# Kernel tuning notes

Measured on AMD Instinct MI355X. Metric: run time of the kernel, lower is better.

Reference implementation:

```python
import jax, jax.numpy as jnp
import numpy as np

B, CIN, COUT, N, T, KT, DTEM, K, D = 16, 32, 64, 1024, 24, 3, 32, 8, 8
TOUT = T - (KT - 1) * 2  # dilated valid conv: 20
NEG = -32767.0  # -2**15 + 1, matches torch small_value


def conv1x1(x, w, b=None):
    # 1x1 Conv2d on NCHW-style [B, C, N, T]
    y = jnp.einsum('bcnt,oc->bont', x, w)
    return y if b is None else y + b[None, :, None, None]


def setup_inputs() -> dict:
    ks = jax.random.split(jax.random.key(0), 24)
    rn = lambda i, s, sc=0.1: jax.random.normal(ks[i], s, dtype=jnp.float32) * sc
    return {
        'x': rn(0, (B, CIN, N, T), 1.0),
        'tem_embedding': rn(1, (B, DTEM, N, T), 0.1),
        'A0': rn(2, (N, N), 0.03), 'A1': rn(3, (N, N), 0.03),
        'A2': rn(4, (N, N), 0.03), 'A3': rn(5, (N, N), 0.03),
        'w_tc': rn(6, (COUT, CIN, 1, KT)), 'b_tc': rn(7, (COUT,)),
        'wq': rn(8, (COUT, COUT + DTEM)), 'bq': rn(9, (COUT,)),
        'wk': rn(10, (COUT, COUT + DTEM)), 'bk': rn(11, (COUT,)),
        'wv': rn(12, (COUT, COUT + DTEM)), 'bv': rn(13, (COUT,)),
        'wo': rn(14, (COUT, COUT)), 'bo': rn(15, (COUT,)),
        'wg0': rn(16, (COUT, 3 * COUT)), 'bg0': rn(17, (COUT,)),
        'wg1': rn(18, (COUT, 3 * COUT)), 'bg1': rn(19, (COUT,)),
        'w_adp': rn(20, (COUT, 2 * COUT)), 'b_adp': rn(21, (COUT,)),
        'w0f': rn(22, (COUT, COUT)),
    }


def reference(x, tem_embedding, A0, A1, A2, A3, w_tc, b_tc, wq, bq, wk, bk, wv, bv,
              wo, bo, wg0, bg0, wg1, bg1, w_adp, b_adp, w0f):
    x = jax.lax.conv_general_dilated(x, w_tc, (1, 1), 'VALID', rhs_dilation=(1, 2),
                                     dimension_numbers=('NCHW', 'OIHW', 'NCHW'))
    x = jax.nn.relu(x + b_tc[None, :, None, None])
    t = x.shape[3]  # TOUT
    # --- TATT: masked multi-head temporal attention ---
    xe = jnp.concatenate([x, tem_embedding[:, :, :, -t:]], axis=1)
    # split channels into K heads of size D (channel-major head layout == torch split/cat)
    q = conv1x1(xe, wq, bq).reshape(B, K, D, N, t)
    k = conv1x1(xe, wk, bk).reshape(B, K, D, N, t)
    v = conv1x1(xe, wv, bv).reshape(B, K, D, N, t)
    att = jnp.einsum('bkdnt,bkdns->bknts', q, k) / jnp.sqrt(jnp.float32(D))
    mask = jnp.tril(jnp.ones((t, t), dtype=bool))  # causal tril mask over time
    att = jax.nn.softmax(jnp.where(mask, att, NEG), axis=-1)
    x = jnp.einsum('bknts,bkdns->bkdnt', att, v).reshape(B, K * D, N, t)
    x = jax.nn.relu(conv1x1(x, wo, bo))
    # --- MGC: multi-hop graph diffusion, order=2, support_len=2, num_graphs=2 ---
    # nconv: out[b,c,w,t] = sum_v x[b,c,v,t] * A[w,v]  (A transposed in original)
    nc = lambda h, A: jnp.einsum('bcvt,wv->bcwt', h, A)
    h0 = jax.nn.relu(conv1x1(jnp.concatenate([x, nc(x, A0), nc(x, A1)], axis=1), wg0, bg0))
    h1 = jax.nn.relu(conv1x1(jnp.concatenate([x, nc(x, A2), nc(x, A3)], axis=1), wg1, bg1))
    # --- micro_fusion: attention over graphs ---
    u = conv1x1(jnp.concatenate([h0, h1], axis=1), w_adp, b_adp)  # [B,C,N,T]
    h = jnp.stack([conv1x1(h0, w0f), conv1x1(h1, w0f)], axis=-1)  # [B,C,N,T,G]
    a = jax.nn.softmax(jnp.einsum('bcntg,bcnt->bntg', h, u), axis=-1)
    return jnp.sum(a[:, None] * h, axis=-1)  # [B,C,N,T]
```

## Files before the change

### kernel.cpp

```cpp
#include <hip/hip_runtime.h>
#include <hip/hip_bf16.h>
#include <stdint.h>

constexpr int BB=16, CIN=32, CO=64, NNODE=1024, TT=24, KTAP=3, DTEM=32, NH=8, HD=8, TO=20;

typedef __attribute__((ext_vector_type(4))) float f32x4;
typedef __attribute__((ext_vector_type(8))) short bf16x8;

__device__ __forceinline__ unsigned short f2bf(float f) {
  union { float f; unsigned u; } v; v.f = f;
  unsigned r = v.u + 0x7FFFu + ((v.u >> 16) & 1u);
  return (unsigned short)(r >> 16);
}
__device__ __forceinline__ float bf2f(unsigned short s) {
  union { unsigned u; float f; } v; v.u = ((unsigned)s) << 16; return v.f;
}

constexpr size_t WADPB_OFF = 0;
constexpr size_t W0FB_OFF  = 16384;
constexpr size_t WG0_OFF   = 163840;
constexpr size_t WG1_OFF   = 188416;
constexpr size_t WTCB_OFF  = 212992;
constexpr size_t WQKVB_OFF = 226304;
constexpr size_t WOB_OFF   = 266240;
constexpr size_t ABF_OFF   = (size_t)1 << 20;
constexpr size_t CHUNK0    = (size_t)12 << 20;

__global__ __launch_bounds__(256) void k_prep_w(
    const float* __restrict__ wtc, const float* __restrict__ wq,
    const float* __restrict__ wk,  const float* __restrict__ wv,
    const float* __restrict__ wo,  const float* __restrict__ wadp,
    const float* __restrict__ w0f, const float* __restrict__ wg0,
    const float* __restrict__ wg1,
    unsigned short* __restrict__ wadpB, unsigned short* __restrict__ w0fB,
    unsigned short* __restrict__ wg0bf, unsigned short* __restrict__ wg1bf,
    unsigned short* __restrict__ wtcB,  unsigned short* __restrict__ wqkvB,
    unsigned short* __restrict__ woB)
{
  int id = blockIdx.x * 256 + threadIdx.x;
  if (id < 8192) {
    wadpB[id] = f2bf(wadp[id]);
  } else if (id < 12288) {
    int j = id - 8192; w0fB[j] = f2bf(w0f[j]);
  } else if (id < 24576) {
    int j = id - 12288; wg0bf[j] = f2bf(wg0[j]);
  } else if (id < 36864) {
    int j = id - 24576; wg1bf[j] = f2bf(wg1[j]);
  } else if (id < 43008) {
    int j = id - 36864; int o = j / 96, k = j % 96, kt = k >> 5, ci = k & 31;
    wtcB[o * 104 + k] = f2bf(wtc[(o * 32 + ci) * 3 + kt]);
  } else if (id < 61440) {
    int j = id - 43008; int r = j / 96, c = j % 96, m = r >> 6, o = r & 63;
    const float* w = (m == 0) ? wq : (m == 1) ? wk : wv;
    wqkvB[r * 104 + c] = f2bf(w[o * 96 + c]);
  } else if (id < 65536) {
    int j = id - 61440;
    woB[(j >> 6) * 72 + (j & 63)] = f2bf(wo[j]);
  }
}

__global__ __launch_bounds__(256) void k_prep_a(
    const float* __restrict__ A0, const float* __restrict__ A1,
    const float* __restrict__ A2, const float* __restrict__ A3,
    unsigned short* __restrict__ Abf)
{
  int idx = blockIdx.x * 256 + threadIdx.x;
  int base = idx * 4;
  if (base >= 4 * 1024 * 1024) return;
  int g = base >> 20; int r = base & 1048575;
  const float* Ag = (g == 0) ? A0 : (g == 1) ? A1 : (g == 2) ? A2 : A3;
  float4 v = *reinterpret_cast<const float4*>(Ag + r);
  ushort4 o;
  o.x = f2bf(v.x); o.y = f2bf(v.y); o.z = f2bf(v.z); o.w = f2bf(v.w);
  *reinterpret_cast<ushort4*>(Abf + base) = o;
}

__global__ __launch_bounds__(256) void k_ttr(
    const float* __restrict__ tem, unsigned short* __restrict__ temT, int b0)
{
  __shared__ __align__(16) unsigned short T[320 * 40];
  const int nb = blockIdx.x, bl = blockIdx.y, b = b0 + bl;
  const int tid = threadIdx.x;
  for (int i = tid; i < 2560; i += 256) {
    int cj = i / 80, r = i % 80, nl = r / 5, q = r % 5;
    float4 v = *reinterpret_cast<const float4*>(
        tem + ((size_t)(b * 32 + cj) * 1024 + nb * 16 + nl) * 24 + 4 + q * 4);
    int row = nl * 20 + q * 4;
    T[(row + 0) * 40 + cj] = f2bf(v.x);
    T[(row + 1) * 40 + cj] = f2bf(v.y);
    T[(row + 2) * 40 + cj] = f2bf(v.z);
    T[(row + 3) * 40 + cj] = f2bf(v.w);
  }
  __syncthreads();
  for (int ch = tid; ch < 1280; ch += 256) {
    int row = ch >> 2, seg = ch & 3;
    *reinterpret_cast<uint4*>(temT + ((size_t)bl * 20480 + nb * 320 + row) * 32 + seg * 8) =
        *reinterpret_cast<const uint4*>(&T[row * 40 + seg * 8]);
  }
}

__global__ __launch_bounds__(256) void k_conv(
    const float* __restrict__ x,
    const unsigned short* __restrict__ wtcB, const float* __restrict__ btc,
    unsigned short* __restrict__ xc, int b0)
{
  __shared__ __align__(16) unsigned short Xs[8 * 24 * 40];
  __shared__ __align__(16) unsigned short Ws[64 * 104];
  __shared__ __align__(16) unsigned short Os[128 * 72];
  const int tid = threadIdx.x, lane = tid & 63, wid = tid >> 6;
  const int wr = wid >> 1, wc = wid & 1;
  const int ptile = blockIdx.x, bl = blockIdx.y, b = b0 + bl;
  const int p0 = ptile * 128, n0 = p0 / 20;

  for (int i = tid; i < 832; i += 256) {
    int row = i / 13, seg = i % 13;
    *reinterpret_cast<uint4*>(&Ws[row * 104 + seg * 8]) =
        *reinterpret_cast<const uint4*>(wtcB + row * 104 + seg * 8);
  }
  for (int i = tid; i < 6144; i += 256) {
    int ci = i / 192, e = i % 192, nl = e / 24, t = e - nl * 24;
    int n = n0 + nl;
    float val = (n < 1024) ? x[((size_t)(b * 32 + ci) * 1024 + n) * 24 + t] : 0.f;
    Xs[(nl * 24 + t) * 40 + ci] = f2bf(val);
  }
  __syncthreads();

  int abase[4];
#pragma unroll
  for (int mi = 0; mi < 4; ++mi) {
    int r = wr * 64 + mi * 16 + (lane & 15);
    int p = p0 + r, n = p / 20, t = p - n * 20;
    abase[mi] = ((n - n0) * 24 + t) * 40 + (lane >> 4) * 8;
  }

  f32x4 acc[4][2];
#pragma unroll
  for (int mi = 0; mi < 4; ++mi)
#pragma unroll
    for (int ni = 0; ni < 2; ++ni) acc[mi][ni] = f32x4{0.f, 0.f, 0.f, 0.f};

#pragma unroll
  for (int kk = 0; kk < 3; ++kk) {
    bf16x8 a[4], bw[2];
#pragma unroll
    for (int mi = 0; mi < 4; ++mi)
      a[mi] = *reinterpret_cast<const bf16x8*>(&Xs[abase[mi] + kk * 80]);
#pragma unroll
    for (int ni = 0; ni < 2; ++ni)
      bw[ni] = *reinterpret_cast<const bf16x8*>(
          &Ws[(wc * 32 + ni * 16 + (lane & 15)) * 104 + kk * 32 + (lane >> 4) * 8]);
#pragma unroll
    for (int mi = 0; mi < 4; ++mi)
#pragma unroll
      for (int ni = 0; ni < 2; ++ni)
        acc[mi][ni] = __builtin_amdgcn_mfma_f32_16x16x32_bf16(a[mi], bw[ni], acc[mi][ni], 0, 0, 0);
  }

#pragma unroll
  for (int ni = 0; ni < 2; ++ni) {
    int col = wc * 32 + ni * 16 + (lane & 15);
    float bias = btc[col];
#pragma unroll
    for (int mi = 0; mi < 4; ++mi)
#pragma unroll
      for (int rr = 0; rr < 4; ++rr) {
        int row = wr * 64 + mi * 16 + (lane >> 4) * 4 + rr;
        Os[row * 72 + col] = f2bf(fmaxf(acc[mi][ni][rr] + bias, 0.f));
      }
  }
  __syncthreads();
  for (int ch = tid; ch < 1024; ch += 256) {
    int row = ch >> 3, seg = ch & 7;
    *reinterpret_cast<uint4*>(xc + ((size_t)bl * 20480 + p0 + row) * 64 + seg * 8) =
        *reinterpret_cast<const uint4*>(&Os[row * 72 + seg * 8]);
  }
}

__global__ __launch_bounds__(256) void k_qkv(
    const unsigned short* __restrict__ xc, const unsigned short* __restrict__ temT,
    const unsigned short* __restrict__ wqkvB,
    const float* __restrict__ bq, const float* __restrict__ bk,
    const float* __restrict__ bv, unsigned short* __restrict__ qkv)
{
  __shared__ __align__(16) unsigned short As[128 * 104];
  __shared__ __align__(16) unsigned short Ws[192 * 104];
  const int tid = threadIdx.x, lane = tid & 63, wid = tid >> 6;
  const int wr = wid >> 1, wc = wid & 1;
  const int ptile = blockIdx.x, bl = blockIdx.y;
  const int p0 = ptile * 128;

  for (int i = tid; i < 1536; i += 256) {
    int row = i / 12, seg = i % 12;
    uint4 v;
    if (seg < 8)
      v = *reinterpret_cast<const uint4*>(xc + ((size_t)bl * 20480 + p0 + row) * 64 + seg * 8);
    else
      v = *reinterpret_cast<const uint4*>(temT + ((size_t)bl * 20480 + p0 + row) * 32 + (seg - 8) * 8);
    *reinterpret_cast<uint4*>(&As[row * 104 + seg * 8]) = v;
  }
  for (int i = tid; i < 2496; i += 256) {
    int row = i / 13, seg = i % 13;
    *reinterpret_cast<uint4*>(&Ws[row * 104 + seg * 8]) =
        *reinterpret_cast<const uint4*>(wqkvB + row * 104 + seg * 8);
  }
  __syncthreads();

  f32x4 acc[4][6];
#pragma unroll
  for (int mi = 0; mi < 4; ++mi)
#pragma unroll
    for (int ni = 0; ni < 6; ++ni) acc[mi][ni] = f32x4{0.f, 0.f, 0.f, 0.f};

#pragma unroll
  for (int kk = 0; kk < 3; ++kk) {
    bf16x8 a[4];
#pragma unroll
    for (int mi = 0; mi < 4; ++mi)
      a[mi] = *reinterpret_cast<const bf16x8*>(
          &As[(wr * 64 + mi * 16 + (lane & 15)) * 104 + kk * 32 + (lane >> 4) * 8]);
#pragma unroll
    for (int ni = 0; ni < 6; ++ni) {
      bf16x8 bw = *reinterpret_cast<const bf16x8*>(
          &Ws[(wc * 96 + ni * 16 + (lane & 15)) * 104 + kk * 32 + (lane >> 4) * 8]);
#pragma unroll
      for (int mi = 0; mi < 4; ++mi)
        acc[mi][ni] = __builtin_amdgcn_mfma_f32_16x16x32_bf16(a[mi], bw, acc[mi][ni], 0, 0, 0);
    }
  }

  for (int p = 0; p < 2; ++p) {
    __syncthreads();
    if (wc == p) {
#pragma unroll
      for (int ni = 0; ni < 6; ++ni) {
        int c = wc * 96 + ni * 16 + (lane & 15);
        int m = c >> 6, chn = c & 63;
        float bias = (m == 0) ? bq[chn] : (m == 1) ? bk[chn] : bv[chn];
        int colp = ni * 16 + (lane & 15);
#pragma unroll
        for (int mi = 0; mi < 4; ++mi)
#pragma unroll
          for (int rr = 0; rr < 4; ++rr) {
            int row = wr * 64 + mi * 16 + (lane >> 4) * 4 + rr;
            As[row * 104 + colp] = f2bf(acc[mi][ni][rr] + bias);
          }
      }
    }
    __syncthreads();
    for (int ch = tid; ch < 1536; ch += 256) {
      int row = ch / 12, seg = ch % 12;
      *reinterpret_cast<uint4*>(qkv + ((size_t)bl * 20480 + p0 + row) * 192 + p * 96 + seg * 8) =
          *reinterpret_cast<const uint4*>(&As[row * 104 + seg * 8]);
    }
  }
}

__global__ __launch_bounds__(256) void k_att(
    const unsigned short* __restrict__ qkv, unsigned short* __restrict__ attout)
{
  const int bx = blockIdx.x;
  const int bl = bx >> 7, nb = bx & 127;
  const int tid = threadIdx.x;
  const int h = tid & 7, nl = (tid >> 3) & 7, tq = tid >> 6;
  const int n = nb * 8 + nl;
  const unsigned short* base = qkv + ((size_t)bl * 20480 + (size_t)n * 20) * 192;
  unsigned short* obase = attout + ((size_t)bl * 20480 + (size_t)n * 20) * 64;
  const float scale = 0.3535533905932738f;

  for (int j = 0; j < 5; ++j) {
    const int t = tq + 4 * j;
    union { uint4 u; unsigned short s[8]; } qr, kr, vr, orr;
    qr.u = *reinterpret_cast<const uint4*>(base + t * 192 + h * 8);
    float q[8];
#pragma unroll
    for (int d = 0; d < 8; ++d) q[d] = bf2f(qr.s[d]) * scale;
    float m = -1e30f, l = 0.f, o[8];
#pragma unroll
    for (int d = 0; d < 8; ++d) o[d] = 0.f;
    for (int s = 0; s <= t; ++s) {
      kr.u = *reinterpret_cast<const uint4*>(base + s * 192 + 64 + h * 8);
      float sc = 0.f;
#pragma unroll
      for (int d = 0; d < 8; ++d) sc += q[d] * bf2f(kr.s[d]);
      float nm = fmaxf(m, sc);
      float w = __expf(m - nm), p = __expf(sc - nm);
      vr.u = *reinterpret_cast<const uint4*>(base + s * 192 + 128 + h * 8);
      l = l * w + p;
#pragma unroll
      for (int d = 0; d < 8; ++d) o[d] = o[d] * w + p * bf2f(vr.s[d]);
      m = nm;
    }
    float inv = 1.f / l;
#pragma unroll
    for (int d = 0; d < 8; ++d) orr.s[d] = f2bf(o[d] * inv);
    *reinterpret_cast<uint4*>(obase + t * 64 + h * 8) = orr.u;
  }
}

__global__ __launch_bounds__(256) void k_wo(
    const unsigned short* __restrict__ attout, const unsigned short* __restrict__ woB,
    const float* __restrict__ bo, unsigned short* __restrict__ x2bf)
{
  __shared__ __align__(16) unsigned short As[128 * 72];
  __shared__ __align__(16) unsigned short Ws[64 * 72];
  const int tid = threadIdx.x, lane = tid & 63, wid = tid >> 6;
  const int wr = wid >> 1, wc = wid & 1;
  const int ptile = blockIdx.x, bl = blockIdx.y;
  const int p0 = ptile * 128;

  for (int i = tid; i < 1024; i += 256) {
    int row = i >> 3, seg = i & 7;
    *reinterpret_cast<uint4*>(&As[row * 72 + seg * 8]) =
        *reinterpret_cast<const uint4*>(attout + ((size_t)bl * 20480 + p0 + row) * 64 + seg * 8);
  }
  for (int i = tid; i < 576; i += 256) {
    int row = i / 9, seg = i % 9;
    *reinterpret_cast<uint4*>(&Ws[row * 72 + seg * 8]) =
        *reinterpret_cast<const uint4*>(woB + row * 72 + seg * 8);
  }
  __syncthreads();

  f32x4 acc[4][2];
#pragma unroll
  for (int mi = 0; mi < 4; ++mi)
#pragma unroll
    for (int ni = 0; ni < 2; ++ni) acc[mi][ni] = f32x4{0.f, 0.f, 0.f, 0.f};

#pragma unroll
  for (int kk = 0; kk < 2; ++kk) {
    bf16x8 a[4], bw[2];
#pragma unroll
    for (int mi = 0; mi < 4; ++mi)
      a[mi] = *reinterpret_cast<const bf16x8*>(
          &As[(wr * 64 + mi * 16 + (lane & 15)) * 72 + kk * 32 + (lane >> 4) * 8]);
#pragma unroll
    for (int ni = 0; ni < 2; ++ni)
      bw[ni] = *reinterpret_cast<const bf16x8*>(
          &Ws[(wc * 32 + ni * 16 + (lane & 15)) * 72 + kk * 32 + (lane >> 4) * 8]);
#pragma unroll
    for (int mi = 0; mi < 4; ++mi)
#pragma unroll
      for (int ni = 0; ni < 2; ++ni)
        acc[mi][ni] = __builtin_amdgcn_mfma_f32_16x16x32_bf16(a[mi], bw[ni], acc[mi][ni], 0, 0, 0);
  }

  __syncthreads();
#pragma unroll
  for (int ni = 0; ni < 2; ++ni) {
    int col = wc * 32 + ni * 16 + (lane & 15);
    float bias = bo[col];
#pragma unroll
    for (int mi = 0; mi < 4; ++mi)
#pragma unroll
      for (int rr = 0; rr < 4; ++rr) {
        int row = wr * 64 + mi * 16 + (lane >> 4) * 4 + rr;
        As[row * 72 + col] = f2bf(fmaxf(acc[mi][ni][rr] + bias, 0.f));
      }
  }
  __syncthreads();
  for (int ch = tid; ch < 1024; ch += 256) {
    int row = ch >> 3, seg = ch & 7;
    int p = p0 + row, n = p / 20, t = p - n * 20;
    *reinterpret_cast<uint4*>(x2bf + ((size_t)(bl * 20 + t) * 1024 + n) * 64 + seg * 8) =
        *reinterpret_cast<const uint4*>(&As[row * 72 + seg * 8]);
  }
}

__global__ __launch_bounds__(256) void k_trx2(
    const unsigned short* __restrict__ x2bf, unsigned short* __restrict__ x2t)
{
  __shared__ __align__(16) unsigned short tile[64 * 72];
  const int nb = blockIdx.x, bt = blockIdx.y;
  const int tid = threadIdx.x;
  for (int ch = tid; ch < 512; ch += 256) {
    int row = ch >> 3, seg = ch & 7;
    *reinterpret_cast<uint4*>(&tile[row * 72 + seg * 8]) =
        *reinterpret_cast<const uint4*>(x2bf + ((size_t)bt * 1024 + nb * 64 + row) * 64 + seg * 8);
  }
  __syncthreads();
  for (int ch = tid; ch < 512; ch += 256) {
    int c = ch >> 3, seg = ch & 7;
    union { unsigned short v[8]; uint4 u; } pk;
#pragma unroll
    for (int j = 0; j < 8; ++j) pk.v[j] = tile[(seg * 8 + j) * 72 + c];
    *reinterpret_cast<uint4*>(x2t + ((size_t)bt * 64 + c) * 1024 + nb * 64 + seg * 8) = pk.u;
  }
}

__global__ __launch_bounds__(256) void k_nconv(
    const unsigned short* __restrict__ Abf,
    const unsigned short* __restrict__ x2t,
    unsigned short* __restrict__ ybf, int NT)
{
  __shared__ __align__(16) unsigned short As[128 * 72];
  __shared__ __align__(16) unsigned short Xs[64 * 72];
  const int wt = blockIdx.x & 7;
  const int btl = blockIdx.x >> 3;
  const int gl = blockIdx.y;
  const int tid = threadIdx.x, lane = tid & 63, wid = tid >> 6;
  const int wr = wid >> 1, wc = wid & 1;
  const unsigned short* Ag = Abf + (size_t)gl * 1024 * 1024 + (size_t)wt * 128 * 1024;
  const unsigned short* Xg = x2t + (size_t)btl * 64 * 1024;

  f32x4 acc[4][2];
#pragma unroll
  for (int mi = 0; mi < 4; ++mi)
#pragma unroll
    for (int ni = 0; ni < 2; ++ni) acc[mi][ni] = f32x4{0.f, 0.f, 0.f, 0.f};

  for (int vb = 0; vb < 1024; vb += 64) {
    __syncthreads();
    for (int ch = tid; ch < 1024; ch += 256) {
      int row = ch >> 3, seg = ch & 7;
      *reinterpret_cast<uint4*>(&As[row * 72 + seg * 8]) =
          *reinterpret_cast<const uint4*>(Ag + (size_t)row * 1024 + vb + seg * 8);
    }
    for (int ch = tid; ch < 512; ch += 256) {
      int row = ch >> 3, seg = ch & 7;
      *reinterpret_cast<uint4*>(&Xs[row * 72 + seg * 8]) =
          *reinterpret_cast<const uint4*>(Xg + (size_t)row * 1024 + vb + seg * 8);
    }
    __syncthreads();
#pragma unroll
    for (int kk = 0; kk < 2; ++kk) {
      bf16x8 a[4], bfr[2];
#pragma unroll
      for (int mi = 0; mi < 4; ++mi)
        a[mi] = *reinterpret_cast<const bf16x8*>(
            &As[(wr * 64 + mi * 16 + (lane & 15)) * 72 + kk * 32 + (lane >> 4) * 8]);
#pragma unroll
      for (int ni = 0; ni < 2; ++ni)
        bfr[ni] = *reinterpret_cast<const bf16x8*>(
            &Xs[(wc * 32 + ni * 16 + (lane & 15)) * 72 + kk * 32 + (lane >> 4) * 8]);
#pragma unroll
      for (int mi = 0; mi < 4; ++mi)
#pragma unroll
        for (int ni = 0; ni < 2; ++ni)
          acc[mi][ni] = __builtin_amdgcn_mfma_f32_16x16x32_bf16(a[mi], bfr[ni], acc[mi][ni], 0, 0, 0);
    }
  }

  __syncthreads();
#pragma unroll
  for (int mi = 0; mi < 4; ++mi)
#pragma unroll
    for (int ni = 0; ni < 2; ++ni)
#pragma unroll
      for (int rr = 0; rr < 4; ++rr) {
        int row = wr * 64 + mi * 16 + (lane >> 4) * 4 + rr;
        int col = wc * 32 + ni * 16 + (lane & 15);
        As[row * 72 + col] = f2bf(acc[mi][ni][rr]);
      }
  __syncthreads();
  const size_t ybase = ((size_t)(gl * NT + btl) * 1024 + wt * 128) * 64;
  for (int ch = tid; ch < 1024; ch += 256) {
    int row = ch >> 3, seg = ch & 7;
    *reinterpret_cast<uint4*>(ybf + ybase + (size_t)row * 64 + seg * 8) =
        *reinterpret_cast<const uint4*>(&As[row * 72 + seg * 8]);
  }
}

__global__ __launch_bounds__(256) void k_wg(
    const unsigned short* __restrict__ x2bf,
    const unsigned short* __restrict__ ybf,
    const unsigned short* __restrict__ wgbf,
    const float* __restrict__ bg,
    unsigned short* __restrict__ hout, int NT)
{
  __shared__ __align__(16) unsigned short As[128 * 72];
  __shared__ __align__(16) unsigned short Ws[64 * 200];
  const int pt = blockIdx.x & 7;
  const int btl = blockIdx.x >> 3;
  const int tid = threadIdx.x, lane = tid & 63, wid = tid >> 6;
  const int wr = wid >> 1, wc = wid & 1;

  for (int ch = tid; ch < 1536; ch += 256) {
    int row = ch / 24, seg = ch % 24;
    *reinterpret_cast<uint4*>(&Ws[row * 200 + seg * 8]) =
        *reinterpret_cast<const uint4*>(wgbf + row * 192 + seg * 8);
  }

  f32x4 acc[4][2];
#pragma unroll
  for (int mi = 0; mi < 4; ++mi)
#pragma unroll
    for (int ni = 0; ni < 2; ++ni) acc[mi][ni] = f32x4{0.f, 0.f, 0.f, 0.f};

  for (int ks = 0; ks < 3; ++ks) {
    const unsigned short* src = (ks == 0)
        ? x2bf + ((size_t)btl * 1024 + pt * 128) * 64
        : ybf + (((size_t)((ks - 1) * NT + btl)) * 1024 + pt * 128) * 64;
    __syncthreads();
    for (int ch = tid; ch < 1024; ch += 256) {
      int row = ch >> 3, seg = ch & 7;
      *reinterpret_cast<uint4*>(&As[row * 72 + seg * 8]) =
          *reinterpret_cast<const uint4*>(src + (size_t)row * 64 + seg * 8);
    }
    __syncthreads();
#pragma unroll
    for (int kk = 0; kk < 2; ++kk) {
      bf16x8 a[4], bfr[2];
#pragma unroll
      for (int mi = 0; mi < 4; ++mi)
        a[mi] = *reinterpret_cast<const bf16x8*>(
            &As[(wr * 64 + mi * 16 + (lane & 15)) * 72 + kk * 32 + (lane >> 4) * 8]);
#pragma unroll
      for (int ni = 0; ni < 2; ++ni)
        bfr[ni] = *reinterpret_cast<const bf16x8*>(
            &Ws[(wc * 32 + ni * 16 + (lane & 15)) * 200 + ks * 64 + kk * 32 + (lane >> 4) * 8]);
#pragma unroll
      for (int mi = 0; mi < 4; ++mi)
#pragma unroll
        for (int ni = 0; ni < 2; ++ni)
          acc[mi][ni] = __builtin_amdgcn_mfma_f32_16x16x32_bf16(a[mi], bfr[ni], acc[mi][ni], 0, 0, 0);
    }
  }

  __syncthreads();
#pragma unroll
  for (int mi = 0; mi < 4; ++mi)
#pragma unroll
    for (int ni = 0; ni < 2; ++ni)
#pragma unroll
      for (int rr = 0; rr < 4; ++rr) {
        int row = wr * 64 + mi * 16 + (lane >> 4) * 4 + rr;
        int col = wc * 32 + ni * 16 + (lane & 15);
        As[row * 72 + col] = f2bf(fmaxf(acc[mi][ni][rr] + bg[col], 0.f));
      }
  __syncthreads();
  const size_t hbase = ((size_t)btl * 1024 + pt * 128) * 64;
  for (int ch = tid; ch < 1024; ch += 256) {
    int row = ch >> 3, seg = ch & 7;
    *reinterpret_cast<uint4*>(hout + hbase + (size_t)row * 64 + seg * 8) =
        *reinterpret_cast<const uint4*>(&As[row * 72 + seg * 8]);
  }
}

__global__ __launch_bounds__(256) void k_fuse2(
    const unsigned short* __restrict__ h0, const unsigned short* __restrict__ h1,
    const unsigned short* __restrict__ wadpB, const unsigned short* __restrict__ w0fB,
    const float* __restrict__ badp, float* __restrict__ otmp)
{
  __shared__ __align__(16) unsigned short As[128 * 136];
  __shared__ __align__(16) unsigned short Bs[64 * 136];
  __shared__ __align__(16) unsigned short Cs[64 * 72];
  const int ntile = blockIdx.x, btl = blockIdx.y;
  const int n0 = ntile * 128;
  const int tid = threadIdx.x, lane = tid & 63, wid = tid >> 6;

  for (int ch = tid; ch < 2048; ch += 256) {
    int half = ch >> 10, r = (ch >> 3) & 127, seg = ch & 7;
    const unsigned short* src = half ? h1 : h0;
    *reinterpret_cast<uint4*>(&As[r * 136 + half * 64 + seg * 8]) =
        *reinterpret_cast<const uint4*>(src + ((size_t)btl * 1024 + n0 + r) * 64 + seg * 8);
  }
  for (int ch = tid; ch < 1024; ch += 256) {
    int r = ch >> 4, seg = ch & 15;
    *reinterpret_cast<uint4*>(&Bs[r * 136 + seg * 8]) =
        *reinterpret_cast<const uint4*>(wadpB + r * 128 + seg * 8);
  }
  for (int ch = tid; ch < 512; ch += 256) {
    int r = ch >> 3, seg = ch & 7;
    *reinterpret_cast<uint4*>(&Cs[r * 72 + seg * 8]) =
        *reinterpret_cast<const uint4*>(w0fB + r * 64 + seg * 8);
  }
  __syncthreads();

  f32x4 aU[2][4], aF0[2][4], aF1[2][4];
#pragma unroll
  for (int mi = 0; mi < 2; ++mi)
#pragma unroll
    for (int ni = 0; ni < 4; ++ni) {
      aU[mi][ni] = f32x4{0.f, 0.f, 0.f, 0.f};
      aF0[mi][ni] = f32x4{0.f, 0.f, 0.f, 0.f};
      aF1[mi][ni] = f32x4{0.f, 0.f, 0.f, 0.f};
    }

  bf16x8 a[2][4];
#pragma unroll
  for (int mi = 0; mi < 2; ++mi)
#pragma unroll
    for (int kk = 0; kk < 4; ++kk)
      a[mi][kk] = *reinterpret_cast<const bf16x8*>(
          &As[(wid * 32 + mi * 16 + (lane & 15)) * 136 + kk * 32 + (lane >> 4) * 8]);

#pragma unroll
  for (int kk = 0; kk < 4; ++kk)
#pragma unroll
    for (int ni = 0; ni < 4; ++ni) {
      bf16x8 bw = *reinterpret_cast<const bf16x8*>(
          &Bs[(ni * 16 + (lane & 15)) * 136 + kk * 32 + (lane >> 4) * 8]);
#pragma unroll
      for (int mi = 0; mi < 2; ++mi)
        aU[mi][ni] = __builtin_amdgcn_mfma_f32_16x16x32_bf16(a[mi][kk], bw, aU[mi][ni], 0, 0, 0);
    }
#pragma unroll
  for (int kk = 0; kk < 2; ++kk)
#pragma unroll
    for (int ni = 0; ni < 4; ++ni) {
      bf16x8 cw = *reinterpret_cast<const bf16x8*>(
          &Cs[(ni * 16 + (lane & 15)) * 72 + kk * 32 + (lane >> 4) * 8]);
#pragma unroll
      for (int mi = 0; mi < 2; ++mi) {
        aF0[mi][ni] = __builtin_amdgcn_mfma_f32_16x16x32_bf16(a[mi][kk], cw, aF0[mi][ni], 0, 0, 0);
        aF1[mi][ni] = __builtin_amdgcn_mfma_f32_16x16x32_bf16(a[mi][kk + 2], cw, aF1[mi][ni], 0, 0, 0);
      }
    }

  float bcol[4];
#pragma unroll
  for (int ni = 0; ni < 4; ++ni) bcol[ni] = badp[ni * 16 + (lane & 15)];

#pragma unroll
  for (int mi = 0; mi < 2; ++mi)
#pragma unroll
    for (int rr = 0; rr < 4; ++rr) {
      float s0 = 0.f, s1 = 0.f;
#pragma unroll
      for (int ni = 0; ni < 4; ++ni) {
        float u = aU[mi][ni][rr] + bcol[ni];
        s0 += aF0[mi][ni][rr] * u;
        s1 += aF1[mi][ni][rr] * u;
      }
#pragma unroll
      for (int off = 1; off < 16; off <<= 1) {
        s0 += __shfl_xor(s0, off);
        s1 += __shfl_xor(s1, off);
      }
      float mmax = fmaxf(s0, s1);
      float e0 = __expf(s0 - mmax), e1 = __expf(s1 - mmax);
      float a0w = e0 / (e0 + e1);
      int row = wid * 32 + mi * 16 + (lane >> 4) * 4 + rr;
      size_t base = ((size_t)btl * 1024 + n0 + row) * 64;
#pragma unroll
      for (int ni = 0; ni < 4; ++ni)
        otmp[base + ni * 16 + (lane & 15)] =
            a0w * aF0[mi][ni][rr] + (1.f - a0w) * aF1[mi][ni][rr];
    }
}

__global__ __launch_bounds__(256) void k_otr(
    const float* __restrict__ otmp, float* __restrict__ out, int b0)
{
  __shared__ __align__(16) float tile[160 * 68];
  const int nb = blockIdx.x;
  const int bl = blockIdx.y;
  const int b = b0 + bl;
  const int tid = threadIdx.x;

  for (int ch = tid; ch < 2560; ch += 256) {
    int t = ch >> 7, rem = ch & 127, nl = rem >> 4, seg = rem & 15;
    *reinterpret_cast<float4*>(&tile[(nl * 20 + t) * 68 + seg * 4]) =
        *reinterpret_cast<const float4*>(
            otmp + ((size_t)(bl * 20 + t) * 1024 + nb * 8 + nl) * 64 + seg * 4);
  }
  __syncthreads();
  for (int ch = tid; ch < 2560; ch += 256) {
    int tq = ch % 5, pair = ch / 5;
    int nl = pair & 7, cc = pair >> 3;
    float4 v;
    v.x = tile[(nl * 20 + tq * 4 + 0) * 68 + cc];
    v.y = tile[(nl * 20 + tq * 4 + 1) * 68 + cc];
    v.z = tile[(nl * 20 + tq * 4 + 2) * 68 + cc];
    v.w = tile[(nl * 20 + tq * 4 + 3) * 68 + cc];
    *reinterpret_cast<float4*>(
        out + ((size_t)(b * 64 + cc) * 1024 + nb * 8 + nl) * 20 + tq * 4) = v;
  }
}

extern "C" void kernel_launch(void* const* d_in, const int* in_sizes, int n_in,
                              void* d_out, int out_size, void* d_ws, size_t ws_size,
                              hipStream_t stream) {
  (void)in_sizes; (void)n_in; (void)out_size;
  const float* x    = (const float*)d_in[0];
  const float* tem  = (const float*)d_in[1];
  const float* A0   = (const float*)d_in[2];
  const float* A1   = (const float*)d_in[3];
  const float* A2   = (const float*)d_in[4];
  const float* A3   = (const float*)d_in[5];
  const float* wtc  = (const float*)d_in[6];
  const float* btc  = (const float*)d_in[7];
  const float* wq   = (const float*)d_in[8];
  const float* bq   = (const float*)d_in[9];
  const float* wk   = (const float*)d_in[10];
  const float* bk   = (const float*)d_in[11];
  const float* wv   = (const float*)d_in[12];
  const float* bv   = (const float*)d_in[13];
  const float* wo   = (const float*)d_in[14];
  const float* bo   = (const float*)d_in[15];
  const float* wg0  = (const float*)d_in[16];
  const float* bg0  = (const float*)d_in[17];
  const float* wg1  = (const float*)d_in[18];
  const float* bg1  = (const float*)d_in[19];
  const float* wadp = (const float*)d_in[20];
  const float* badp = (const float*)d_in[21];
  const float* w0f  = (const float*)d_in[22];

  char* ws = (char*)d_ws;
  unsigned short* wadpB = (unsigned short*)(ws + WADPB_OFF);
  unsigned short* w0fB  = (unsigned short*)(ws + W0FB_OFF);
  unsigned short* wg0bf = (unsigned short*)(ws + WG0_OFF);
  unsigned short* wg1bf = (unsigned short*)(ws + WG1_OFF);
  unsigned short* wtcB  = (unsigned short*)(ws + WTCB_OFF);
  unsigned short* wqkvB = (unsigned short*)(ws + WQKVB_OFF);
  unsigned short* woB   = (unsigned short*)(ws + WOB_OFF);
  unsigned short* Abf   = (unsigned short*)(ws + ABF_OFF);

  const size_t SBH  = (size_t)20480 * 64 * 2;
  const size_t SBT  = (size_t)20480 * 32 * 2;
  const size_t SBQ  = (size_t)20480 * 192 * 2;
  const size_t SBY  = 2 * SBH;
  int CB = 1;
  {
    const int cands[4] = {16, 8, 4, 2};
    for (int i = 0; i < 4; ++i) {
      size_t need = CHUNK0 + (size_t)cands[i] * (SBH + SBT + SBQ + SBY + SBH);
      if (need <= ws_size) { CB = cands[i]; break; }
    }
  }
  const int NT = CB * TO;
  const size_t XC0  = CHUNK0;
  const size_t TT0  = XC0 + (size_t)CB * SBH;
  const size_t QKV0 = TT0 + (size_t)CB * SBT;
  const size_t Y0   = QKV0 + (size_t)CB * SBQ;
  const size_t H00  = Y0 + (size_t)CB * SBY;
  unsigned short* xc     = (unsigned short*)(ws + XC0);
  unsigned short* temT   = (unsigned short*)(ws + TT0);
  unsigned short* qkvbuf = (unsigned short*)(ws + QKV0);
  unsigned short* attout = (unsigned short*)(ws + XC0);
  unsigned short* x2bf   = (unsigned short*)(ws + QKV0);
  unsigned short* x2t    = (unsigned short*)(ws + QKV0 + (size_t)CB * SBH);
  unsigned short* ybuf   = (unsigned short*)(ws + Y0);
  unsigned short* h0     = (unsigned short*)(ws + H00);
  unsigned short* h1     = x2t;
  float* otmp            = (float*)(ws + Y0);
  float* out = (float*)d_out;

  k_prep_w<<<dim3(256), dim3(256), 0, stream>>>(wtc, wq, wk, wv, wo, wadp, w0f,
                                                wg0, wg1, wadpB, w0fB, wg0bf, wg1bf,
                                                wtcB, wqkvB, woB);
  k_prep_a<<<dim3(4096), dim3(256), 0, stream>>>(A0, A1, A2, A3, Abf);

  for (int b0 = 0; b0 < BB; b0 += CB) {
    k_ttr<<<dim3(64, CB), dim3(256), 0, stream>>>(tem, temT, b0);
    k_conv<<<dim3(160, CB), dim3(256), 0, stream>>>(x, wtcB, btc, xc, b0);
    k_qkv<<<dim3(160, CB), dim3(256), 0, stream>>>(xc, temT, wqkvB, bq, bk, bv, qkvbuf);
    k_att<<<dim3(CB * 128), dim3(256), 0, stream>>>(qkvbuf, attout);
    k_wo<<<dim3(160, CB), dim3(256), 0, stream>>>(attout, woB, bo, x2bf);
    k_trx2<<<dim3(16, NT), dim3(256), 0, stream>>>(x2bf, x2t);
    k_nconv<<<dim3(8 * NT, 2), dim3(256), 0, stream>>>(Abf, x2t, ybuf, NT);
    k_wg<<<dim3(8 * NT), dim3(256), 0, stream>>>(x2bf, ybuf, wg0bf, bg0, h0, NT);
    k_nconv<<<dim3(8 * NT, 2), dim3(256), 0, stream>>>(Abf + 2 * 1024 * 1024, x2t, ybuf, NT);
    k_wg<<<dim3(8 * NT), dim3(256), 0, stream>>>(x2bf, ybuf, wg1bf, bg1, h1, NT);
    k_fuse2<<<dim3(8, NT), dim3(256), 0, stream>>>(h0, h1, wadpB, w0fB, badp, otmp);
    k_otr<<<dim3(128, CB), dim3(256), 0, stream>>>(otmp, out, b0);
  }
}
```

Baseline: 993.3 us.

## Widen nconv tiles to 128x128 with direct-to-LDS loads, XOR swizzle and block remap

The graph diffusion GEMM kernel now computes a 128x128 output tile (two bt slices per block) instead of 128x64. This halves the number of times the adjacency tile is reloaded and raises MFMA work per LDS load. Operands are staged with global_load_lds directly into XOR-swizzled unpadded LDS, and block indices are remapped so that blocks sharing an A tile run close together. The cost is more accumulator registers, an extra LDS buffer for the epilogue, and a grid half as large, which may reduce occupancy.

New measurement: 844.8 us. 15.0% less time.

```diff
diff --git a/kernel.cpp b/kernel.cpp
--- a/kernel.cpp
+++ b/kernel.cpp
@@ -14,6 +14,11 @@
 }
 __device__ __forceinline__ float bf2f(unsigned short s) {
   union { unsigned u; float f; } v; v.u = ((unsigned)s) << 16; return v.f;
+}
+__device__ __forceinline__ void gl_lds16(const unsigned short* g, unsigned short* l) {
+  __builtin_amdgcn_global_load_lds(
+      (const __attribute__((address_space(1))) unsigned int*)g,
+      (__attribute__((address_space(3))) unsigned int*)l, 16, 0, 0);
 }
 
 constexpr size_t WADPB_OFF = 0;
@@ -392,71 +397,84 @@
     const unsigned short* __restrict__ x2t,
     unsigned short* __restrict__ ybf, int NT)
 {
-  __shared__ __align__(16) unsigned short As[128 * 72];
-  __shared__ __align__(16) unsigned short Xs[64 * 72];
-  const int wt = blockIdx.x & 7;
-  const int btl = blockIdx.x >> 3;
+  __shared__ __align__(16) unsigned short As[128 * 64];
+  __shared__ __align__(16) unsigned short Bs[128 * 64];
+  __shared__ __align__(16) unsigned short Cs[128 * 72];
+  const int nwg = gridDim.x;
+  const int chunk = nwg >> 3;
+  const int bx = blockIdx.x;
+  const int v = (bx & 7) * chunk + (bx >> 3);
+  const int wt = v & 7;
+  const int ntile = v >> 3;
   const int gl = blockIdx.y;
   const int tid = threadIdx.x, lane = tid & 63, wid = tid >> 6;
   const int wr = wid >> 1, wc = wid & 1;
+  const int lrow = lane >> 3, lslot = lane & 7;
   const unsigned short* Ag = Abf + (size_t)gl * 1024 * 1024 + (size_t)wt * 128 * 1024;
-  const unsigned short* Xg = x2t + (size_t)btl * 64 * 1024;
-
-  f32x4 acc[4][2];
+  const unsigned short* Bg = x2t + (size_t)ntile * 128 * 1024;
+
+  f32x4 acc[4][4];
 #pragma unroll
   for (int mi = 0; mi < 4; ++mi)
 #pragma unroll
-    for (int ni = 0; ni < 2; ++ni) acc[mi][ni] = f32x4{0.f, 0.f, 0.f, 0.f};
+    for (int ni = 0; ni < 4; ++ni) acc[mi][ni] = f32x4{0.f, 0.f, 0.f, 0.f};
 
   for (int vb = 0; vb < 1024; vb += 64) {
     __syncthreads();
+#pragma unroll
+    for (int j = 0; j < 4; ++j) {
+      int r = wid * 32 + j * 8 + lrow;
+      int so = (lslot ^ (r & 7)) << 3;
+      gl_lds16(Ag + (size_t)r * 1024 + vb + so, As + (wid * 32 + j * 8) * 64);
+      gl_lds16(Bg + (size_t)r * 1024 + vb + so, Bs + (wid * 32 + j * 8) * 64);
+    }
+    __syncthreads();
+#pragma unroll
+    for (int kk = 0; kk < 2; ++kk) {
+      const int hi = lane >> 4;
+      bf16x8 a[4], bfr[4];
+#pragma unroll
+      for (int mi = 0; mi < 4; ++mi) {
+        int row = wr * 64 + mi * 16 + (lane & 15);
+        a[mi] = *reinterpret_cast<const bf16x8*>(
+            &As[row * 64 + (((kk * 4 + hi) ^ (row & 7)) << 3)]);
+      }
+#pragma unroll
+      for (int ni = 0; ni < 4; ++ni) {
+        int row = wc * 64 + ni * 16 + (lane & 15);
+        bfr[ni] = *reinterpret_cast<const bf16x8*>(
+            &Bs[row * 64 + (((kk * 4 + hi) ^ (row & 7)) << 3)]);
+      }
+#pragma unroll
+      for (int mi = 0; mi < 4; ++mi)
+#pragma unroll
+        for (int ni = 0; ni < 4; ++ni)
+          acc[mi][ni] = __builtin_amdgcn_mfma_f32_16x16x32_bf16(a[mi], bfr[ni], acc[mi][ni], 0, 0, 0);
+    }
+  }
+
+  for (int h = 0; h < 2; ++h) {
+    __syncthreads();
+    if (wc == h) {
+#pragma unroll
+      for (int mi = 0; mi < 4; ++mi)
+#pragma unroll
+        for (int ni = 0; ni < 4; ++ni)
+#pragma unroll
+          for (int rr = 0; rr < 4; ++rr) {
+            int row = wr * 64 + mi * 16 + (lane >> 4) * 4 + rr;
+            int col = ni * 16 + (lane & 15);
+            Cs[row * 72 + col] = f2bf(acc[mi][ni][rr]);
+          }
+    }
+    __syncthreads();
+    const int btl = ntile * 2 + h;
+    const size_t ybase = ((size_t)(gl * NT + btl) * 1024 + wt * 128) * 64;
     for (int ch = tid; ch < 1024; ch += 256) {
       int row = ch >> 3, seg = ch & 7;
-      *reinterpret_cast<uint4*>(&As[row * 72 + seg * 8]) =
-          *reinterpret_cast<const uint4*>(Ag + (size_t)row * 1024 + vb + seg * 8);
-    }
-    for (int ch = tid; ch < 512; ch += 256) {
-      int row = ch >> 3, seg = ch & 7;
-      *reinterpret_cast<uint4*>(&Xs[row * 72 + seg * 8]) =
-          *reinterpret_cast<const uint4*>(Xg + (size_t)row * 1024 + vb + seg * 8);
-    }
-    __syncthreads();
-#pragma unroll
-    for (int kk = 0; kk < 2; ++kk) {
-      bf16x8 a[4], bfr[2];
-#pragma unroll
-      for (int mi = 0; mi < 4; ++mi)
-        a[mi] = *reinterpret_cast<const bf16x8*>(
-            &As[(wr * 64 + mi * 16 + (lane & 15)) * 72 + kk * 32 + (lane >> 4) * 8]);
-#pragma unroll
-      for (int ni = 0; ni < 2; ++ni)
-        bfr[ni] = *reinterpret_cast<const bf16x8*>(
-            &Xs[(wc * 32 + ni * 16 + (lane & 15)) * 72 + kk * 32 + (lane >> 4) * 8]);
-#pragma unroll
-      for (int mi = 0; mi < 4; ++mi)
-#pragma unroll
-        for (int ni = 0; ni < 2; ++ni)
-          acc[mi][ni] = __builtin_amdgcn_mfma_f32_16x16x32_bf16(a[mi], bfr[ni], acc[mi][ni], 0, 0, 0);
-    }
-  }
-
-  __syncthreads();
-#pragma unroll
-  for (int mi = 0; mi < 4; ++mi)
-#pragma unroll
-    for (int ni = 0; ni < 2; ++ni)
-#pragma unroll
-      for (int rr = 0; rr < 4; ++rr) {
-        int row = wr * 64 + mi * 16 + (lane >> 4) * 4 + rr;
-        int col = wc * 32 + ni * 16 + (lane & 15);
-        As[row * 72 + col] = f2bf(acc[mi][ni][rr]);
-      }
-  __syncthreads();
-  const size_t ybase = ((size_t)(gl * NT + btl) * 1024 + wt * 128) * 64;
-  for (int ch = tid; ch < 1024; ch += 256) {
-    int row = ch >> 3, seg = ch & 7;
-    *reinterpret_cast<uint4*>(ybf + ybase + (size_t)row * 64 + seg * 8) =
-        *reinterpret_cast<const uint4*>(&As[row * 72 + seg * 8]);
+      *reinterpret_cast<uint4*>(ybf + ybase + (size_t)row * 64 + seg * 8) =
+          *reinterpret_cast<const uint4*>(&Cs[row * 72 + seg * 8]);
+    }
   }
 }
 
@@ -748,9 +766,9 @@
     k_att<<<dim3(CB * 128), dim3(256), 0, stream>>>(qkvbuf, attout);
     k_wo<<<dim3(160, CB), dim3(256), 0, stream>>>(attout, woB, bo, x2bf);
     k_trx2<<<dim3(16, NT), dim3(256), 0, stream>>>(x2bf, x2t);
-    k_nconv<<<dim3(8 * NT, 2), dim3(256), 0, stream>>>(Abf, x2t, ybuf, NT);
+    k_nconv<<<dim3((NT / 2) * 8, 2), dim3(256), 0, stream>>>(Abf, x2t, ybuf, NT);
     k_wg<<<dim3(8 * NT), dim3(256), 0, stream>>>(x2bf, ybuf, wg0bf, bg0, h0, NT);
-    k_nconv<<<dim3(8 * NT, 2), dim3(256), 0, stream>>>(Abf + 2 * 1024 * 1024, x2t, ybuf, NT);
+    k_nconv<<<dim3((NT / 2) * 8, 2), dim3(256), 0, stream>>>(Abf + 2 * 1024 * 1024, x2t, ybuf, NT);
     k_wg<<<dim3(8 * NT), dim3(256), 0, stream>>>(x2bf, ybuf, wg1bf, bg1, h1, NT);
     k_fuse2<<<dim3(8, NT), dim3(256), 0, stream>>>(h0, h1, wadpB, w0fB, badp, otmp);
     k_otr<<<dim3(128, CB), dim3(256), 0, stream>>>(otmp, out, b0);
```
